# Performance work log

Hardware: AMD Instinct MI355X
Metric: run time of the kernel (lower is better)

Reference implementation:

```python
import jax, jax.numpy as jnp
import numpy as np

EPS = 1e-05
N = 8192


def setup_inputs() -> dict:
    key = jax.random.key(0)
    k1, k2 = jax.random.split(key)
    params = jax.random.normal(k1, (3,), dtype=jnp.float32) * 0.1
    # sparse-ish symmetric 0/1 adjacency, float32 like the torch buffer
    a = (jax.random.uniform(k2, (N, N)) < 0.005).astype(jnp.float32)
    graph = jnp.maximum(a, a.T)
    return {"params": params, "graph": graph}


def reference(params, graph):
    alpha, beta, sigma = params[0], params[1], params[2]
    n = graph.shape[0]
    # p == 0 => sum_degrees(v) is just the degree (row sum) of v
    deg = jnp.sum(graph, axis=1)                       # [n]
    s = alpha * deg[:, None] + beta * deg[None, :] + sigma   # [n, n]
    p = 1.0 / (1.0 + jnp.exp(s))                        # logistic prob
    ll = jnp.where(graph == 1.0,
                   jnp.log(p + EPS),
                   jnp.log(1.0 - p + EPS))
    # loop runs over i <= j: upper triangle including diagonal
    upper = jnp.triu(jnp.ones((n, n), dtype=bool))
    likelihood = jnp.sum(jnp.where(upper, ll, 0.0))
    return -likelihood
```

## Files before the change

### kernel.cpp

```cpp
#include <hip/hip_runtime.h>

#define N 8192
#define EPS 1e-5f
#define LOG2E 1.4426950408889634f
#define LN2d  0.6931471805599453

#define TR 64
#define TC 256
#define NBJ 32
#define NBI 128
#define RPW 16
#define CAPW 512
#define SEG_W 4096
#define NTILES 2112
#define NSEG (NTILES * 4)
#define RMAX 512
#define NA 32
#define NDR 1024
#define EDGE0 (NA + 1 + NDR)
#define NFB 1024

static const size_t OFF_ACC = 0;
static const size_t OFF_DEG = 4096;
static const size_t OFF_CNT = OFF_DEG + (size_t)N * 4;
static const size_t OFF_EDG = OFF_CNT + (size_t)NSEG * 4;
static const size_t WS_NEED = OFF_EDG + (size_t)NSEG * SEG_W * 4;

__device__ __forceinline__ unsigned mbcnt64(unsigned long long m) {
    return __builtin_amdgcn_mbcnt_hi((unsigned)(m >> 32),
           __builtin_amdgcn_mbcnt_lo((unsigned)m, 0u));
}

__global__ __launch_bounds__(256) void k_pass1(const float* __restrict__ g,
        float* __restrict__ deg, unsigned* __restrict__ cnt,
        unsigned* __restrict__ edges, const int segmode) {
    const int bj = (int)blockIdx.x & (NBJ - 1);
    const int bi = (int)blockIdx.x >> 5;
    if (bi > 4 * bj + 3) return;
    const int r0 = bi * TR, c0 = bj * TC;
    const int wave = threadIdx.x >> 6, lane = threadIdx.x & 63;
    const int aid = 2 * bj * (bj + 1) + bi;

    __shared__ float    scol[TC];
    __shared__ unsigned buf[4][CAPW];
    scol[threadIdx.x] = 0.f;
    __syncthreads();

    const int c = c0 + lane * 4;
    const int rbase = r0 + wave * RPW;
    const float* __restrict__ gp = g + (size_t)rbase * N + c;
    unsigned* __restrict__ myseg = edges + ((size_t)aid * 4 + wave) * SEG_W;
    unsigned wc = 0, wflushed = 0;
    float ca0 = 0.f, ca1 = 0.f, ca2 = 0.f, ca3 = 0.f;

#define EMIT(BB, PRED, OFFv) \
    if (BB) { if (segmode && (PRED)) buf[wave][wc + mbcnt64(BB)] = etag | (OFFv); \
        const unsigned p_ = __popcll(BB); wc += p_; rsum += p_; }

#define FLUSHCHK \
    if (segmode && wc > (unsigned)(CAPW - 256)) { \
        for (unsigned t_ = lane; t_ < wc; t_ += 64) myseg[wflushed + t_] = buf[wave][t_]; \
        wflushed += wc; wc = 0; }

    if (r0 + TR <= c0) {
        #pragma unroll 4
        for (int k = 0; k < RPW; ++k) {
            const float4 v = *reinterpret_cast<const float4*>(gp + (size_t)k * N);
            FLUSHCHK
            ca0 += v.x; ca1 += v.y; ca2 += v.z; ca3 += v.w;
            const unsigned long long b0 = __ballot(v.x != 0.f);
            const unsigned long long b1 = __ballot(v.y != 0.f);
            const unsigned long long b2 = __ballot(v.z != 0.f);
            const unsigned long long b3 = __ballot(v.w != 0.f);
            if (b0 | b1 | b2 | b3) {
                const int gr = rbase + k;
                const unsigned etag = ((unsigned)gr << 16) | (unsigned)c;
                unsigned rsum = 0;
                EMIT(b0, v.x != 0.f, 0u)
                EMIT(b1, v.y != 0.f, 1u)
                EMIT(b2, v.z != 0.f, 2u)
                EMIT(b3, v.w != 0.f, 3u)
                if (lane == 0) atomicAdd(&deg[gr], (float)rsum);
            }
        }
    } else {
        for (int k = 0; k < RPW; ++k) {
            const int gr = rbase + k;
            const float4 v = *reinterpret_cast<const float4*>(gp + (size_t)k * N);
            FLUSHCHK
            const bool a0 = (v.x != 0.f) && (c + 0 >= gr);
            const bool a1 = (v.y != 0.f) && (c + 1 >= gr);
            const bool a2 = (v.z != 0.f) && (c + 2 >= gr);
            const bool a3 = (v.w != 0.f) && (c + 3 >= gr);
            ca0 += (c + 0 > gr) ? v.x : 0.f;
            ca1 += (c + 1 > gr) ? v.y : 0.f;
            ca2 += (c + 2 > gr) ? v.z : 0.f;
            ca3 += (c + 3 > gr) ? v.w : 0.f;
            const unsigned long long b0 = __ballot(a0);
            const unsigned long long b1 = __ballot(a1);
            const unsigned long long b2 = __ballot(a2);
            const unsigned long long b3 = __ballot(a3);
            if (b0 | b1 | b2 | b3) {
                const unsigned etag = ((unsigned)gr << 16) | (unsigned)c;
                unsigned rsum = 0;
                EMIT(b0, a0, 0u)
                EMIT(b1, a1, 1u)
                EMIT(b2, a2, 2u)
                EMIT(b3, a3, 3u)
                if (lane == 0) atomicAdd(&deg[gr], (float)rsum);
            }
        }
    }
#undef EMIT
#undef FLUSHCHK

    if (segmode) {
        for (unsigned t = lane; t < wc; t += 64) myseg[wflushed + t] = buf[wave][t];
        if (lane == 0) cnt[aid * 4 + wave] = wflushed + wc;
    }
    if (ca0 != 0.f) atomicAdd(&scol[lane * 4 + 0], ca0);
    if (ca1 != 0.f) atomicAdd(&scol[lane * 4 + 1], ca1);
    if (ca2 != 0.f) atomicAdd(&scol[lane * 4 + 2], ca2);
    if (ca3 != 0.f) atomicAdd(&scol[lane * 4 + 3], ca3);
    __syncthreads();
    const float sv = scol[threadIdx.x];
    if (sv != 0.f) atomicAdd(&deg[c0 + threadIdx.x], sv);
}

__global__ __launch_bounds__(256) void k_ll(const float* __restrict__ g,
        const float* __restrict__ deg, const float* __restrict__ params,
        const unsigned* __restrict__ cnt, const unsigned* __restrict__ edges,
        double* __restrict__ accv, const int segmode) {
    __shared__ double wsum[4];
    __shared__ float  srange[8];
    __shared__ int    hist[RMAX];
    __shared__ float  dchunk[256];
    const int tid = threadIdx.x;
    const int wv = tid >> 6, ln = tid & 63;
    const int b = blockIdx.x;
    const float alpha = params[0], beta = params[1], sigma = params[2];
    const float a2 = alpha * LOG2E, b2 = beta * LOG2E, s2 = sigma * LOG2E;
    double dlocal = 0.0;

#define F2(X, Y) __builtin_amdgcn_logf(1.00001f - __builtin_amdgcn_rcpf(1.f + \
        __builtin_amdgcn_exp2f(fmaf(a2, (X), fmaf(b2, (Y), s2)))))

    if (b < EDGE0) {
        if (segmode) {
            float mn = 3.0e38f, mx = -3.0e38f;
            for (int j = tid; j < N; j += 256) {
                const float d = deg[j];
                mn = fminf(mn, d); mx = fmaxf(mx, d);
            }
            #pragma unroll
            for (int off = 32; off; off >>= 1) {
                mn = fminf(mn, __shfl_xor(mn, off));
                mx = fmaxf(mx, __shfl_xor(mx, off));
            }
            if (ln == 0) { srange[wv] = mn; srange[4 + wv] = mx; }
            __syncthreads();
            mn = fminf(fminf(srange[0], srange[1]), fminf(srange[2], srange[3]));
            mx = fmaxf(fmaxf(srange[4], srange[5]), fmaxf(srange[6], srange[7]));
            const int dmin = (int)mn;
            const int R = (int)mx - dmin + 1;

            if (b < NA) {
                if (R <= RMAX) {
                    const int j0 = b * 256;
                    for (int i = tid; i < R; i += 256) hist[i] = 0;
                    __syncthreads();
                    for (int i = tid; i < j0; i += 256)
                        atomicAdd(&hist[(int)deg[i] - dmin], 1);
                    dchunk[tid] = deg[j0 + tid];
                    __syncthreads();
                    const float dj = dchunk[tid];
                    double accA = 0.0;
                    for (int i = 0; i < tid; ++i) {
                        const float di = dchunk[i];
                        accA += (double)(F2(di, dj) - F2(dj, di));
                    }
                    for (int d = 0; d < R; ++d) {
                        const int c = hist[d];
                        if (c) {
                            const float dd = (float)(dmin + d);
                            accA += (double)c * (double)(F2(dd, dj) - F2(dj, dd));
                        }
                    }
                    dlocal = accA * 0.5 * LN2d;
                }
            } else if (b == NA) {
                if (R <= RMAX) {
                    for (int i = tid; i < R; i += 256) hist[i] = 0;
                    __syncthreads();
                    for (int i = tid; i < N; i += 256)
                        atomicAdd(&hist[(int)deg[i] - dmin], 1);
                    __syncthreads();
                    double accT = 0.0;
                    const int RR = R * R;
                    for (int cell = tid; cell < RR; cell += 256) {
                        const int a = cell / R, bb = cell - a * R;
                        const long long c = (long long)hist[a] * hist[bb];
                        if (c) accT += (double)c *
                            (double)F2((float)(dmin + a), (float)(dmin + bb));
                    }
                    for (int a = tid; a < R; a += 256) {
                        if (hist[a]) accT += (double)hist[a] *
                            (double)F2((float)(dmin + a), (float)(dmin + a));
                    }
                    dlocal = accT * 0.5 * LN2d;
                }
            } else {
                if (R > RMAX) {
                    const int db = b - NA - 1;
                    float ls = 0.f;
                    for (int q = 0; q < 4; ++q) {
                        const int r1 = db + q * NDR, r2 = N - 1 - r1;
                        const float dr1 = deg[r1], dr2 = deg[r2];
                        for (int j = r1 + tid; j < N; j += 256) ls += F2(dr1, deg[j]);
                        for (int j = r2 + tid; j < N; j += 256) ls += F2(dr2, deg[j]);
                    }
                    dlocal = (double)ls * LN2d;
                }
            }
        }
    } else if (b < EDGE0 + NTILES) {
        if (!segmode) return;
        const int aid = b - EDGE0;
        float local = 0.f;
        for (int w = 0; w < 4; ++w) {
            const unsigned n = cnt[aid * 4 + w];
            const unsigned* __restrict__ seg = edges + ((size_t)aid * 4 + w) * SEG_W;
            for (unsigned t = tid; t < n; t += 256) {
                const unsigned e = seg[t];
                const float di = deg[e >> 16];
                const float dj = deg[e & 0xffffu];
                const float s = fmaf(alpha, di, fmaf(beta, dj, sigma));
                const float p = __fdividef(1.f, 1.f + __expf(s));
                local += __logf(p + EPS) - __logf(1.f - p + EPS);
            }
        }
        dlocal = (double)local;
    } else {
        if (segmode) return;
        const int rb = b - EDGE0 - NTILES;
        for (int q = 0; q < 8; ++q) {
            const int i = rb * 8 + q;
            const float base = fmaf(alpha, deg[i], sigma);
            float rl = 0.f;
            for (int j = i + tid; j < N; j += 256) {
                const float s = fmaf(beta, deg[j], base);
                const float p = __fdividef(1.f, 1.f + __expf(s));
                const float gv = g[(size_t)i * N + j];
                rl += (gv != 0.f) ? __logf(p + EPS) : __logf(1.f - p + EPS);
            }
            dlocal += (double)rl;
        }
    }
#undef F2

    #pragma unroll
    for (int off = 32; off; off >>= 1) dlocal += __shfl_xor(dlocal, off);
    if (ln == 0) wsum[wv] = dlocal;
    __syncthreads();
    if (tid == 0) {
        const double t = (wsum[0] + wsum[1]) + (wsum[2] + wsum[3]);
        if (t != 0.0) atomicAdd(&accv[(b & 63) * 8], t);
    }
}

__global__ void k_final(const double* __restrict__ accv, float* __restrict__ out) {
    double v = accv[threadIdx.x * 8];
    #pragma unroll
    for (int off = 32; off; off >>= 1) v += __shfl_xor(v, off);
    if (threadIdx.x == 0) out[0] = (float)(-v);
}

extern "C" void kernel_launch(void* const* d_in, const int* in_sizes, int n_in,
                              void* d_out, int out_size, void* d_ws, size_t ws_size,
                              hipStream_t stream) {
    const float* params = (const float*)d_in[0];
    const float* graph  = (const float*)d_in[1];
    float* out = (float*)d_out;

    char* ws = (char*)d_ws;
    double*   accv  = (double*)(ws + OFF_ACC);
    float*    deg   = (float*)(ws + OFF_DEG);
    unsigned* cnt   = (unsigned*)(ws + OFF_CNT);
    unsigned* edges = (unsigned*)(ws + OFF_EDG);
    const int segmode = (ws_size >= WS_NEED) ? 1 : 0;

    hipMemsetAsync(ws, 0, OFF_DEG + (size_t)N * 4, stream);
    k_pass1<<<NBI * NBJ, 256, 0, stream>>>(graph, deg, cnt, edges, segmode);
    const int llgrid = segmode ? (EDGE0 + NTILES) : (EDGE0 + NTILES + NFB);
    k_ll<<<llgrid, 256, 0, stream>>>(graph, deg, params, cnt, edges, accv, segmode);
    k_final<<<1, 64, 0, stream>>>(accv, out);
}
```

Measured before the change: 72.43 us.

## Replace degree-histogram dense term with shared-memory F2 lookup table and ballot prefix counts

The dense log(1-p) sum over the upper triangle is now computed in the 32 fast-path blocks using a precomputed R×R table of F2 values in shared memory. Each block's within-chunk prefix counts per degree come from wave ballots and popcounts instead of a 256-step pairwise loop. The separate whole-histogram block is removed, so the block indices shift by one. This cuts transcendental evaluations per thread, but it lowers the degree-range threshold to 100, so wider ranges fall back to the slow brute-force path. It also uses about 40KB of shared memory per block, which may reduce occupancy.

```diff
diff --git a/kernel.cpp b/kernel.cpp
--- a/kernel.cpp
+++ b/kernel.cpp
@@ -14,10 +14,10 @@
 #define SEG_W 4096
 #define NTILES 2112
 #define NSEG (NTILES * 4)
-#define RMAX 512
+#define RMAX2 100
 #define NA 32
 #define NDR 1024
-#define EDGE0 (NA + 1 + NDR)
+#define EDGE0 (NA + NDR)
 #define NFB 1024
 
 static const size_t OFF_ACC = 0;
@@ -131,10 +131,11 @@
         const float* __restrict__ deg, const float* __restrict__ params,
         const unsigned* __restrict__ cnt, const unsigned* __restrict__ edges,
         double* __restrict__ accv, const int segmode) {
+    __shared__ float  ftbl[RMAX2 * RMAX2];
+    __shared__ unsigned long long msk[RMAX2][4];
+    __shared__ int    Ph[RMAX2];
     __shared__ double wsum[4];
     __shared__ float  srange[8];
-    __shared__ int    hist[RMAX];
-    __shared__ float  dchunk[256];
     const int tid = threadIdx.x;
     const int wv = tid >> 6, ln = tid & 63;
     const int b = blockIdx.x;
@@ -164,63 +165,43 @@
             const int dmin = (int)mn;
             const int R = (int)mx - dmin + 1;
 
-            if (b < NA) {
-                if (R <= RMAX) {
-                    const int j0 = b * 256;
-                    for (int i = tid; i < R; i += 256) hist[i] = 0;
-                    __syncthreads();
-                    for (int i = tid; i < j0; i += 256)
-                        atomicAdd(&hist[(int)deg[i] - dmin], 1);
-                    dchunk[tid] = deg[j0 + tid];
-                    __syncthreads();
-                    const float dj = dchunk[tid];
-                    double accA = 0.0;
-                    for (int i = 0; i < tid; ++i) {
-                        const float di = dchunk[i];
-                        accA += (double)(F2(di, dj) - F2(dj, di));
-                    }
-                    for (int d = 0; d < R; ++d) {
-                        const int c = hist[d];
-                        if (c) {
-                            const float dd = (float)(dmin + d);
-                            accA += (double)c * (double)(F2(dd, dj) - F2(dj, dd));
-                        }
-                    }
-                    dlocal = accA * 0.5 * LN2d;
-                }
-            } else if (b == NA) {
-                if (R <= RMAX) {
-                    for (int i = tid; i < R; i += 256) hist[i] = 0;
-                    __syncthreads();
-                    for (int i = tid; i < N; i += 256)
-                        atomicAdd(&hist[(int)deg[i] - dmin], 1);
-                    __syncthreads();
-                    double accT = 0.0;
-                    const int RR = R * R;
-                    for (int cell = tid; cell < RR; cell += 256) {
-                        const int a = cell / R, bb = cell - a * R;
-                        const long long c = (long long)hist[a] * hist[bb];
-                        if (c) accT += (double)c *
-                            (double)F2((float)(dmin + a), (float)(dmin + bb));
-                    }
-                    for (int a = tid; a < R; a += 256) {
-                        if (hist[a]) accT += (double)hist[a] *
-                            (double)F2((float)(dmin + a), (float)(dmin + a));
-                    }
-                    dlocal = accT * 0.5 * LN2d;
-                }
-            } else {
-                if (R > RMAX) {
-                    const int db = b - NA - 1;
-                    float ls = 0.f;
-                    for (int q = 0; q < 4; ++q) {
-                        const int r1 = db + q * NDR, r2 = N - 1 - r1;
-                        const float dr1 = deg[r1], dr2 = deg[r2];
-                        for (int j = r1 + tid; j < N; j += 256) ls += F2(dr1, deg[j]);
-                        for (int j = r2 + tid; j < N; j += 256) ls += F2(dr2, deg[j]);
-                    }
-                    dlocal = (double)ls * LN2d;
-                }
+            if (b < NA && R <= RMAX2) {
+                const int j0 = b * 256;
+                for (int i = tid; i < RMAX2; i += 256) Ph[i] = 0;
+                __syncthreads();
+                for (int i = tid; i < j0; i += 256)
+                    atomicAdd(&Ph[(int)deg[i] - dmin], 1);
+                const int ct = (int)deg[j0 + tid] - dmin;
+                for (int a = 0; a < R; ++a) {
+                    const unsigned long long m = __ballot(ct == a);
+                    if (ln == 0) msk[a][wv] = m;
+                }
+                for (int cell = tid; cell < R * R; cell += 256) {
+                    const int a = cell / R, bb = cell - a * R;
+                    ftbl[cell] = F2((float)(dmin + a), (float)(dmin + bb));
+                }
+                __syncthreads();
+                const unsigned long long lmask =
+                    (ln == 0) ? 0ull : (~0ull >> (64 - ln));
+                double acc = 0.0;
+                for (int a = 0; a < R; ++a) {
+                    int c2 = Ph[a];
+                    for (int w2 = 0; w2 < wv; ++w2) c2 += __popcll(msk[a][w2]);
+                    c2 += __popcll(msk[a][wv] & lmask);
+                    acc += (double)((float)c2 * ftbl[a * R + ct]);
+                }
+                acc += (double)ftbl[ct * R + ct];
+                dlocal = acc * LN2d;
+            } else if (b >= NA && R > RMAX2) {
+                const int db = b - NA;
+                float ls = 0.f;
+                for (int q = 0; q < 4; ++q) {
+                    const int r1 = db + q * NDR, r2 = N - 1 - r1;
+                    const float dr1 = deg[r1], dr2 = deg[r2];
+                    for (int j = r1 + tid; j < N; j += 256) ls += F2(dr1, deg[j]);
+                    for (int j = r2 + tid; j < N; j += 256) ls += F2(dr2, deg[j]);
+                }
+                dlocal = (double)ls * LN2d;
             }
         }
     } else if (b < EDGE0 + NTILES) {
```

Result: slower. 79.19 us (+9.3%).
